# Kernel tuning notes

Hardware: AMD Instinct MI355X
Metric: run time of the kernel (lower is better)

Reference implementation:

```python
import jax, jax.numpy as jnp
import numpy as np


def _glorot(key, shape):
    lim = np.sqrt(6.0 / (shape[-2] + shape[-1])).astype(np.float32)
    return jax.random.uniform(key, shape, jnp.float32, -lim, lim)


def setup_inputs() -> dict:
    key = jax.random.key(0)
    B, F, K, L = 8192, 256, 32768, 4
    H = 2 * F          # CouplingLayer(feat_size, feat_size * 2) hidden width
    half = F // 2      # affine coupling transforms half the features
    ks = jax.random.split(key, 6)
    return {
        "inputs": jax.random.normal(ks[0], (B, F), jnp.float32),
        "W1": _glorot(ks[1], (L, half, H)),
        "b1": jnp.zeros((L, H), jnp.float32),
        "Ws": _glorot(ks[2], (L, H, half)),
        "bs": jnp.zeros((L, half), jnp.float32),
        "Wt": _glorot(ks[3], (L, H, half)),
        "bt": jnp.zeros((L, half), jnp.float32),
        "prior": _glorot(ks[4], (K, F)),  # VQ codebook, GlorotUniform init as in source
    }


def _forward_flow(x, W1, b1, Ws, bs, Wt, bt):
    """Stack of affine coupling layers; returns (y, log|det J|) per sample."""
    L = W1.shape[0]
    jac = jnp.zeros((x.shape[0],), x.dtype)
    for l in range(L):  # small fixed layer count
        xa, xb = jnp.split(x, 2, axis=1)                 # [B, F/2] each
        h = jax.nn.relu(xa @ W1[l] + b1[l])              # [B, 2F]
        s_raw = h @ Ws[l] + bs[l]                        # [B, F/2]
        s = s_raw if l == L - 1 else jnp.tanh(s_raw)     # last layer: tf.identity
        t = h @ Wt[l] + bt[l]
        yb = xb * jnp.exp(s) + t
        jac = jac + jnp.sum(s, axis=1)
        x = jnp.concatenate([yb, xa], axis=1)            # swap halves for mixing
    return x, jac


def reference(inputs, W1, b1, Ws, bs, Wt, bt, prior):
    sg = jax.lax.stop_gradient
    x, jac = _forward_flow(inputs, W1, b1, Ws, bs, Wt, bt)   # [B, F], [B]
    # pairwise squared distance to codebook: [B, K]
    na = jnp.sum(x * x, axis=1, keepdims=True)               # [B, 1]
    nb = jnp.sum(prior * prior, axis=1)[None, :]             # [1, K]
    d = jnp.maximum(na - 2.0 * (x @ prior.T) + nb, 0.0)      # [B, K]
    target_ind = jnp.argmin(d, axis=1)                       # [B]
    target = prior[target_ind]                               # gather, [B, F]
    loss_1 = jnp.mean(jnp.sum((x - sg(target)) ** 2, axis=1) / 2)
    loss_2 = jnp.mean(jnp.sum((sg(x) - target) ** 2, axis=1) / 2)
    loss = loss_1 + 0.25 * loss_2 - jnp.mean(jac)
    return x, loss
```

## Files before the change

kernel.cpp:

```cpp
#include <hip/hip_runtime.h>
#include <hip/hip_fp8.h>
#include <stdint.h>

#define NB     8192
#define NF     256
#define NHALF  128
#define NHID   512
#define NLAY   4
#define NK     32768

#define SX     (1.0f / 16.0f)
#define SP     (256.0f)

typedef __attribute__((ext_vector_type(8))) short bf16x8;
typedef __attribute__((ext_vector_type(4))) float f32x4;
typedef __attribute__((ext_vector_type(8))) int i32x8;

static __device__ __forceinline__ unsigned short f2bf(float f) {
  union { float f; unsigned int u; } v; v.f = f;
  return (unsigned short)((v.u + 0x7FFFu + ((v.u >> 16) & 1u)) >> 16);
}
static __device__ __forceinline__ float bf2f(unsigned short u) {
  union { unsigned int u; float f; } v; v.u = ((unsigned int)u) << 16; return v.f;
}
static __device__ __forceinline__ unsigned char f2fp8(float f) {
  __hip_fp8_e4m3 q(f);
  return (unsigned char)q.__x;
}
static __device__ __forceinline__ float fp82f(unsigned char b) {
  __hip_fp8_e4m3 q; q.__x = b; return (float)q;
}

static __device__ __forceinline__ void load_lds16(const void* g, void* l) {
  __builtin_amdgcn_global_load_lds(
      (const __attribute__((address_space(1))) unsigned int*)g,
      (__attribute__((address_space(3))) unsigned int*)l, 16, 0, 0);
}

static __device__ __forceinline__ unsigned long long packsi(float v, int idx) {
  unsigned int b = __float_as_uint(v);
  b = (b & 0x80000000u) ? ~b : (b | 0x80000000u);
  return ((unsigned long long)b << 32) | (unsigned int)(~(unsigned int)idx);
}

static __device__ __forceinline__ float fast_tanh(float x) {
  const float xc = fminf(fmaxf(x, -15.f), 15.f);
  const float e2 = __expf(2.f * xc);
  return 1.f - 2.f / (e2 + 1.f);
}

static __device__ __forceinline__ int swadr(int kseg, int nrows, int row, int kin) {
  return (kseg * nrows + row) * 64 + (((kin >> 3) ^ (row & 7)) * 8) + (kin & 7);
}

static __device__ __forceinline__ void stage_seg(
    int g, unsigned short* dst,
    const unsigned short* __restrict__ W1T,
    const unsigned short* __restrict__ W2I,
    int wave, int lane, int bxr, int hswap)
{
  const int l = g / 24, s = g % 24;
  const int nc = ((s / 3) + bxr) & 7;
  const int t = s % 3;
  if (t == 0) {
    const unsigned short* W1l = W1T + (size_t)l * (NHID * NHALF) + (size_t)nc * 64 * 128;
#pragma unroll
    for (int u = 0; u < 2; u++) {
      const int chb = (u * 8 + wave) * 64;
      const int ch = chb + lane;
      const int kseg = ch >> 9, cs = ch & 511;
      const int row = cs >> 3, cc = (cs & 7) ^ (row & 7);
      load_lds16(W1l + (size_t)row * 128 + kseg * 64 + cc * 8, dst + chb * 8);
    }
  } else {
    const int half = (t - 1) ^ hswap;
    const unsigned short* W2l = W2I + (size_t)l * (NF * NHID) + nc * 64 + half * 32;
#pragma unroll
    for (int u = 0; u < 2; u++) {
      const int chb = (u * 8 + wave) * 64;
      const int ch = chb + lane;
      const int row = ch >> 2;
      const int cc = (ch & 3) ^ ((row >> 1) & 3);
      load_lds16(W2l + (size_t)row * NHID + cc * 8, dst + chb * 8);
    }
  }
}

__global__ __launch_bounds__(512, 2)
void flow_all(const float* __restrict__ in,
              const unsigned short* __restrict__ W1T,
              const unsigned short* __restrict__ W2I,
              const float* __restrict__ b1A,
              const float* __restrict__ bsA,
              const float* __restrict__ btA,
              float* __restrict__ xout,
              unsigned char* __restrict__ xf8,
              float* __restrict__ jac)
{
  __shared__ __align__(16) unsigned short Xb[2][32 * 128];
  __shared__ __align__(16) unsigned short Hs[32 * 64];
  __shared__ __align__(16) unsigned short Bs[5][8192];
  __shared__ float b1s[NLAY * NHID];
  __shared__ float bss[NLAY * NHALF];
  __shared__ float bts[NLAY * NHALF];
  __shared__ float jlds[4][32];
  const int tid = threadIdx.x;
  const int lane = tid & 63, wave = tid >> 6;
  const int rg = wave >> 2, cg = wave & 3;
  const int q = lane >> 4, c = lane & 15;
  const int m0 = blockIdx.x * 32;
  const int bxr = blockIdx.x & 7;
  const int hswap = (blockIdx.x >> 3) & 1;

  stage_seg(0, Bs[0], W1T, W2I, wave, lane, bxr, hswap);

#pragma unroll
  for (int v = 0; v < 4; v++) {
    const int t4 = tid + v * 512;
    const int row = t4 >> 6, f4 = t4 & 63;
    const float4 d = *(const float4*)(in + (size_t)(m0 + row) * NF + f4 * 4);
    unsigned short* dst = Xb[f4 >> 5];
    const int feat = (f4 & 31) * 4;
    const float vals[4] = {d.x, d.y, d.z, d.w};
#pragma unroll
    for (int u = 0; u < 4; u++) {
      const int fe = feat + u;
      dst[swadr(fe >> 6, 32, row, fe & 63)] = f2bf(vals[u]);
    }
  }

#pragma unroll
  for (int v = 0; v < 4; v++) b1s[tid + v * 512] = b1A[tid + v * 512];
  bss[tid] = bsA[tid];
  bts[tid] = btA[tid];

  stage_seg(1, Bs[1], W1T, W2I, wave, lane, bxr, hswap);
  stage_seg(2, Bs[2], W1T, W2I, wave, lane, bxr, hswap);
  stage_seg(3, Bs[3], W1T, W2I, wave, lane, bxr, hswap);

  float jr[4] = {0.f, 0.f, 0.f, 0.f};
  bf16x8 af1[4];
  const f32x4 z = {0.f, 0.f, 0.f, 0.f};
  f32x4 acc2[4];

  for (int gs = 0; gs < 96; gs++) {
    if (gs < 93)
      asm volatile("s_waitcnt vmcnt(6) lgkmcnt(0)\n\ts_barrier" ::: "memory");
    else if (gs == 93)
      asm volatile("s_waitcnt vmcnt(4) lgkmcnt(0)\n\ts_barrier" ::: "memory");
    else if (gs == 94)
      asm volatile("s_waitcnt vmcnt(2) lgkmcnt(0)\n\ts_barrier" ::: "memory");
    else
      asm volatile("s_waitcnt vmcnt(0) lgkmcnt(0)\n\ts_barrier" ::: "memory");

    if (gs + 4 < 96) stage_seg(gs + 4, Bs[(gs + 4) % 5], W1T, W2I, wave, lane, bxr, hswap);

    const int l = gs / 24, s = gs % 24, typ = s % 3;
    const int nc8 = ((s / 3) + bxr) & 7;
    const unsigned short* B = Bs[gs % 5];
    unsigned short* XA = Xb[l & 1];
    unsigned short* XB = Xb[1 - (l & 1)];

    if (typ == 0) {
      if (s == 0) {
#pragma unroll
        for (int kw = 0; kw < 4; kw++) {
          const int kch = kw * 4 + q;
          af1[kw] = *(const bf16x8*)(XA + ((kch >> 3) * 32 + rg * 16 + c) * 64 +
                                     (((kch & 7) ^ (c & 7)) * 8));
        }
#pragma unroll
        for (int j = 0; j < 4; j++) acc2[j] = z;
      }
      f32x4 acc1 = z;
      const int rb = cg * 16 + c;
#pragma unroll
      for (int kw = 0; kw < 4; kw++) {
        const int kseg = kw >> 1, g = (kw & 1) * 4 + q;
        const bf16x8 bf = *(const bf16x8*)(B + (kseg * 64 + rb) * 64 + ((g ^ (rb & 7)) * 8));
        acc1 = __builtin_amdgcn_mfma_f32_16x16x32_bf16(af1[kw], bf, acc1, 0, 0, 0);
      }
      const int hc = cg * 16 + c;
      const float bb = b1s[l * NHID + nc8 * 64 + hc];
#pragma unroll
      for (int r = 0; r < 4; r++) {
        float v = acc1[r] + bb;
        v = v > 0.f ? v : 0.f;
        Hs[swadr(0, 32, rg * 16 + 4 * q + r, hc)] = f2bf(v);
      }
    } else {
      const int half = (typ - 1) ^ hswap;
      const bf16x8 afh = *(const bf16x8*)(Hs + (rg * 16 + c) * 64 +
                                          (((half * 4 + q) ^ (c & 7)) * 8));
#pragma unroll
      for (int j = 0; j < 4; j++) {
        const int rb = cg * 64 + 16 * j + c;
        const bf16x8 bf = *(const bf16x8*)(B + rb * 32 + ((q ^ ((rb >> 1) & 3)) * 8));
        acc2[j] = __builtin_amdgcn_mfma_f32_16x16x32_bf16(afh, bf, acc2[j], 0, 0, 0);
      }
    }

    if (s == 23) {
      const int parity = c & 1;
      const int lastl = (l == NLAY - 1);
      const float* bsl = bss + l * NHALF;
      const float* btl = bts + l * NHALF;
#pragma unroll
      for (int j = 0; j < 4; j++) {
        const int col = cg * 64 + 16 * j + c;
#pragma unroll
        for (int r = 0; r < 4; r++) {
          const float val = acc2[j][r];
          const float oth = __shfl_xor(val, 1);
          if (!parity) {
            const int feat = col >> 1;
            float sv = val + bsl[feat];
            if (!lastl) sv = fast_tanh(sv);
            const float t = oth + btl[feat];
            const int row = rg * 16 + 4 * q + r;
            const int xaddr = swadr(feat >> 6, 32, row, feat & 63);
            const float xb = bf2f(XB[xaddr]);
            const float yb = xb * __expf(sv) + t;
            jr[r] += sv;
            XB[xaddr] = f2bf(yb);
            if (l >= 2) {
              const int k = lastl ? feat : (NHALF + feat);
              const size_t grow = (size_t)(m0 + row) * NF;
              xout[grow + k] = yb;
              xf8[(size_t)(m0 + row) * 256 + k] = f2fp8(yb * SX);
            }
          }
        }
      }
    }
  }

#pragma unroll
  for (int r = 0; r < 4; r++) {
    float v = jr[r];
    v += __shfl_xor(v, 1); v += __shfl_xor(v, 2);
    v += __shfl_xor(v, 4); v += __shfl_xor(v, 8);
    if (c == 0) jlds[cg][rg * 16 + 4 * q + r] = v;
  }
  __syncthreads();
  if (tid < 32)
    jac[m0 + tid] = jlds[0][tid] + jlds[1][tid] + jlds[2][tid] + jlds[3][tid];
}

__global__ __launch_bounds__(256, 2)
void vq_argmax(const unsigned char* __restrict__ X8,
               const unsigned char* __restrict__ P8,
               const float* __restrict__ nbh,
               unsigned long long* __restrict__ gbest)
{
  __shared__ __align__(16) unsigned char Bs[2][64 * 256];
  const int tid = threadIdx.x;
  const int lane = tid & 63, wave = tid >> 6;
  const int y = blockIdx.x & 15;
  const int m0 = (blockIdx.x >> 4) * 256;
  const int q = lane >> 4, c = lane & 15;
  const int mw = m0 + wave * 64;
  const int one = 0x7F7F7F7F;

  i32x8 af[4][2];
#pragma unroll
  for (int i = 0; i < 4; i++) {
    const unsigned char* xr = X8 + (size_t)(mw + 16 * i + c) * 256 + q * 32;
#pragma unroll
    for (int h = 0; h < 2; h++) {
      const int4 lo = *(const int4*)(xr + h * 128);
      const int4 hi = *(const int4*)(xr + h * 128 + 16);
      af[i][h] = (i32x8){lo.x, lo.y, lo.z, lo.w, hi.x, hi.y, hi.z, hi.w};
    }
  }

  float bestv[16];
  int besti[16];
#pragma unroll
  for (int t = 0; t < 16; t++) { bestv[t] = -1e30f; besti[t] = 0; }

  {
    const int n0s = y * 2048;
#pragma unroll
    for (int u = 0; u < 4; u++) {
      const int chb = (u * 4 + wave) * 64;
      const int ch = chb + lane;
      const int row = ch >> 4, gslot = ch & 15;
      load_lds16(P8 + (size_t)(n0s + row) * 256 + (gslot ^ (row & 15)) * 16,
                 Bs[0] + chb * 16);
    }
  }

  for (int nt = 0; nt < 32; nt++) {
    const int n0 = y * 2048 + nt * 64;
    __syncthreads();

    float nbr[4];
#pragma unroll
    for (int j = 0; j < 4; j++) nbr[j] = nbh[n0 + 16 * j + c];

    if (nt + 1 < 32) {
      const int n0s = n0 + 64;
      unsigned char* dst = Bs[(nt + 1) & 1];
#pragma unroll
      for (int u = 0; u < 4; u++) {
        const int chb = (u * 4 + wave) * 64;
        const int ch = chb + lane;
        const int row = ch >> 4, gslot = ch & 15;
        load_lds16(P8 + (size_t)(n0s + row) * 256 + (gslot ^ (row & 15)) * 16,
                   dst + chb * 16);
      }
    }

    const unsigned char* Bt = Bs[nt & 1];
    f32x4 acc[4][4];
#pragma unroll
    for (int i = 0; i < 4; i++)
#pragma unroll
      for (int j = 0; j < 4; j++)
        acc[i][j] = (f32x4){-nbr[j], -nbr[j], -nbr[j], -nbr[j]};

#pragma unroll
    for (int j = 0; j < 4; j++) {
      const unsigned char* base = Bt + (16 * j + c) * 256;
#pragma unroll
      for (int h = 0; h < 2; h++) {
        const int4 b0 = *(const int4*)(base + ((8 * h + 2 * q)     ^ c) * 16);
        const int4 b1 = *(const int4*)(base + ((8 * h + 2 * q + 1) ^ c) * 16);
        const i32x8 bf = (i32x8){b0.x, b0.y, b0.z, b0.w, b1.x, b1.y, b1.z, b1.w};
#pragma unroll
        for (int i = 0; i < 4; i++)
          acc[i][j] = __builtin_amdgcn_mfma_scale_f32_16x16x128_f8f6f4(
              af[i][h], bf, acc[i][j], 0, 0, 0, one, 0, one);
      }
    }

#pragma unroll
    for (int j = 0; j < 4; j++) {
      const int col = n0 + 16 * j + c;
#pragma unroll
      for (int i = 0; i < 4; i++)
#pragma unroll
        for (int r = 0; r < 4; r++) {
          const float sc = acc[i][j][r];
          const int t = i * 4 + r;
          if (sc > bestv[t]) { bestv[t] = sc; besti[t] = col; }
        }
    }
  }

#pragma unroll
  for (int t = 0; t < 16; t++) {
    float lv = bestv[t]; int li = besti[t];
#pragma unroll
    for (int mk = 8; mk >= 1; mk >>= 1) {
      const float ov = __shfl_xor(lv, mk);
      const int oi = __shfl_xor(li, mk);
      if (ov > lv || (ov == lv && oi < li)) { lv = ov; li = oi; }
    }
    if (c == 0) {
      const int row = mw + 16 * (t >> 2) + q * 4 + (t & 3);
      atomicMax(&gbest[row], packsi(lv, li));
    }
  }
}

__global__ void prep_all(const float* __restrict__ W1,
                         const float* __restrict__ Ws,
                         const float* __restrict__ Wt,
                         const float* __restrict__ prior,
                         unsigned short* __restrict__ W1T,
                         unsigned short* __restrict__ W2I,
                         unsigned char* __restrict__ p8,
                         float* __restrict__ nbh,
                         unsigned long long* __restrict__ gbest,
                         float* __restrict__ accum)
{
  __shared__ float ts[64 * 65];
  const int bx = blockIdx.x;
  const int tid = threadIdx.x;
  if (bx < 2048) {
    const int k = bx * 16 + (tid >> 4);
    const int l16 = tid & 15;
    float s = 0.f;
#pragma unroll
    for (int v = 0; v < 4; v++) {
      const int off = (v * 16 + l16) * 4;
      const float4 d = *(const float4*)(prior + (size_t)k * NF + off);
      uchar4 o;
      o.x = f2fp8(d.x * SP); o.y = f2fp8(d.y * SP);
      o.z = f2fp8(d.z * SP); o.w = f2fp8(d.w * SP);
      *(uchar4*)(p8 + (size_t)k * 256 + off) = o;
      const float q0 = fp82f(o.x), q1 = fp82f(o.y), q2 = fp82f(o.z), q3 = fp82f(o.w);
      s += q0 * q0 + q1 * q1 + q2 * q2 + q3 * q3;
    }
#pragma unroll
    for (int mk = 8; mk >= 1; mk >>= 1) s += __shfl_xor(s, mk);
    if (l16 == 0) nbh[k] = 0.5f * s * (SX / SP);
  } else if (bx < 2112) {
    const int job = bx - 2048;
    const int l = job >> 4, t = job & 15;
    const int k0 = (t >> 3) * 64, n0 = (t & 7) * 64;
    const float* src = W1 + (size_t)l * NHALF * NHID;
#pragma unroll
    for (int v = 0; v < 16; v++) {
      const int e = tid + v * 256;
      const int kk = e >> 6, nn = e & 63;
      ts[kk * 65 + nn] = src[(size_t)(k0 + kk) * NHID + n0 + nn];
    }
    __syncthreads();
    unsigned short* dst = W1T + (size_t)l * NHID * NHALF;
#pragma unroll
    for (int v = 0; v < 16; v++) {
      const int e = tid + v * 256;
      const int nn = e >> 6, kk = e & 63;
      dst[(size_t)(n0 + nn) * NHALF + k0 + kk] = f2bf(ts[kk * 65 + nn]);
    }
  } else if (bx < 2240) {
    const int job = bx - 2112;
    const int l = job >> 5, rem = job & 31;
    const int b = rem >> 4;
    const int k0 = ((rem >> 1) & 7) * 64;
    const int f0 = (rem & 1) * 64;
    const float* src = (b ? Wt : Ws) + (size_t)l * NHID * NHALF;
#pragma unroll
    for (int v = 0; v < 16; v++) {
      const int e = tid + v * 256;
      const int kk = e >> 6, nn = e & 63;
      ts[kk * 65 + nn] = src[(size_t)(k0 + kk) * NHALF + f0 + nn];
    }
    __syncthreads();
#pragma unroll
    for (int v = 0; v < 16; v++) {
      const int e = tid + v * 256;
      const int nn = e >> 6, kk = e & 63;
      W2I[((size_t)l * NF + 2 * (f0 + nn) + b) * NHID + k0 + kk] = f2bf(ts[kk * 65 + nn]);
    }
  } else {
    const int idx = (bx - 2240) * 256 + tid;
    if (idx < NB) gbest[idx] = 0ull;
    if (idx < 4) accum[idx] = 0.f;
  }
}

__global__ void vq_finalize(const float* __restrict__ X,
                            const float* __restrict__ prior,
                            const unsigned long long* __restrict__ gbest,
                            const float* __restrict__ jac,
                            float* __restrict__ accum,
                            float* __restrict__ loss)
{
  const int wave = threadIdx.x >> 6, lane = threadIdx.x & 63;
  const int gw = blockIdx.x * 4 + wave;
  float accd = 0.f, accj = 0.f;
  for (int r = 0; r < 8; r++) {
    const int row = gw * 8 + r;
    const unsigned int idx = ~(unsigned int)(gbest[row]);
    const float* x = X + (size_t)row * NF;
    const float* p = prior + (size_t)idx * NF;
#pragma unroll
    for (int u = 0; u < 4; u++) {
      const int d = lane + u * 64;
      const float df = x[d] - p[d];
      accd += df * df;
    }
    if (lane == 0) accj += jac[row];
  }
#pragma unroll
  for (int mk = 32; mk >= 1; mk >>= 1) {
    accd += __shfl_xor(accd, mk);
    accj += __shfl_xor(accj, mk);
  }
  __shared__ float sd[4], sj[4];
  if (lane == 0) { sd[wave] = accd; sj[wave] = accj; }
  __syncthreads();
  if (threadIdx.x == 0) {
    atomicAdd(&accum[0], sd[0] + sd[1] + sd[2] + sd[3]);
    atomicAdd(&accum[1], sj[0] + sj[1] + sj[2] + sj[3]);
    __threadfence();
    const unsigned int t = atomicAdd((unsigned int*)&accum[2], 1u);
    if (t == 255u) {
      const float d = atomicAdd(&accum[0], 0.f);
      const float jv = atomicAdd(&accum[1], 0.f);
      loss[0] = 1.25f * (0.5f * d / (float)NB) - jv / (float)NB;
    }
  }
}

extern "C" void kernel_launch(void* const* d_in, const int* in_sizes, int n_in,
                              void* d_out, int out_size, void* d_ws, size_t ws_size,
                              hipStream_t stream)
{
  (void)in_sizes; (void)n_in; (void)out_size; (void)ws_size;
  const float* inputs = (const float*)d_in[0];
  const float* W1 = (const float*)d_in[1];
  const float* b1 = (const float*)d_in[2];
  const float* Ws = (const float*)d_in[3];
  const float* bs = (const float*)d_in[4];
  const float* Wt = (const float*)d_in[5];
  const float* bt = (const float*)d_in[6];
  const float* prior = (const float*)d_in[7];

  char* p = (char*)d_ws;
  auto alloc = [&](size_t bytes) { char* r = p; p += (bytes + 255) & ~(size_t)255; return r; };
  unsigned short* W1T  = (unsigned short*)alloc((size_t)NLAY * NHID * NHALF * 2);
  unsigned short* W2I  = (unsigned short*)alloc((size_t)NLAY * NF * NHID * 2);
  unsigned char* P8    = (unsigned char*)alloc((size_t)NK * 256);
  float* NBH           = (float*)alloc((size_t)NK * 4);
  unsigned char* XF8   = (unsigned char*)alloc((size_t)NB * 256);
  float* JAC           = (float*)alloc((size_t)NB * 4);
  unsigned long long* GBEST = (unsigned long long*)alloc((size_t)NB * 8);
  float* ACC           = (float*)alloc(256);

  float* xout = (float*)d_out;
  float* loss = xout + (size_t)NB * NF;

  prep_all<<<dim3(2272), 256, 0, stream>>>(
      W1, Ws, Wt, prior, W1T, W2I, P8, NBH, GBEST, ACC);

  flow_all<<<dim3(NB / 32), 512, 0, stream>>>(
      inputs, W1T, W2I, b1, bs, bt, xout, XF8, JAC);

  vq_argmax<<<dim3(32 * 16), 256, 0, stream>>>(XF8, P8, NBH, GBEST);
  vq_finalize<<<dim3(256), 256, 0, stream>>>(xout, prior, GBEST, JAC, ACC, loss);
}
```

Before: 257.0 us.

## Fuse hidden-layer GEMMs in registers via transposed MFMA, coarsen weight staging

Computes the first GEMM transposed (weights as the A operand, activations as B) so each lane's output fragment can be packed directly into the A operand of the second GEMM. This removes the Hs shared-memory round trip and the step that split the second GEMM into halves. The 96 fine-grained steps become 32 chunks, each staging the W1 block and the full W2 block together. Buffering changes from a 5-deep ring to a double buffer with an extra barrier per chunk. The cost is less prefetch depth and more LDS per stage.

```diff
diff --git a/kernel.cpp b/kernel.cpp
--- a/kernel.cpp
+++ b/kernel.cpp
@@ -53,36 +53,32 @@
   return (kseg * nrows + row) * 64 + (((kin >> 3) ^ (row & 7)) * 8) + (kin & 7);
 }
 
-static __device__ __forceinline__ void stage_seg(
+static __device__ __forceinline__ int g1swz(int row) {
+  return (row & 15) ^ ((row & 8) >> 1);
+}
+
+static __device__ __forceinline__ void stage_chunk(
     int g, unsigned short* dst,
     const unsigned short* __restrict__ W1T,
     const unsigned short* __restrict__ W2I,
-    int wave, int lane, int bxr, int hswap)
+    int wave, int lane, int bxr)
 {
-  const int l = g / 24, s = g % 24;
-  const int nc = ((s / 3) + bxr) & 7;
-  const int t = s % 3;
-  if (t == 0) {
-    const unsigned short* W1l = W1T + (size_t)l * (NHID * NHALF) + (size_t)nc * 64 * 128;
-#pragma unroll
-    for (int u = 0; u < 2; u++) {
-      const int chb = (u * 8 + wave) * 64;
-      const int ch = chb + lane;
-      const int kseg = ch >> 9, cs = ch & 511;
-      const int row = cs >> 3, cc = (cs & 7) ^ (row & 7);
-      load_lds16(W1l + (size_t)row * 128 + kseg * 64 + cc * 8, dst + chb * 8);
-    }
-  } else {
-    const int half = (t - 1) ^ hswap;
-    const unsigned short* W2l = W2I + (size_t)l * (NF * NHID) + nc * 64 + half * 32;
-#pragma unroll
-    for (int u = 0; u < 2; u++) {
-      const int chb = (u * 8 + wave) * 64;
-      const int ch = chb + lane;
-      const int row = ch >> 2;
-      const int cc = (ch & 3) ^ ((row >> 1) & 3);
-      load_lds16(W2l + (size_t)row * NHID + cc * 8, dst + chb * 8);
-    }
+  const int l = g >> 3;
+  const int nc = ((g & 7) + bxr) & 7;
+  const unsigned short* W1l = W1T + (size_t)l * (NHID * NHALF) + (size_t)nc * 64 * 128;
+#pragma unroll
+  for (int u = 0; u < 2; u++) {
+    const int ch = (u * 8 + wave) * 64 + lane;
+    const int row = ch >> 4, sl = ch & 15;
+    load_lds16(W1l + (size_t)row * 128 + (sl ^ g1swz(row)) * 8, dst + ch * 8);
+  }
+  const unsigned short* W2l = W2I + (size_t)l * (NF * NHID) + nc * 64;
+#pragma unroll
+  for (int u = 0; u < 4; u++) {
+    const int ch = (u * 8 + wave) * 64 + lane;
+    const int col = ch >> 3, sl = ch & 7;
+    load_lds16(W2l + (size_t)col * NHID + ((sl ^ (col & 7)) * 8),
+               dst + 8192 + ch * 8);
   }
 }
 
@@ -98,8 +94,7 @@
               float* __restrict__ jac)
 {
   __shared__ __align__(16) unsigned short Xb[2][32 * 128];
-  __shared__ __align__(16) unsigned short Hs[32 * 64];
-  __shared__ __align__(16) unsigned short Bs[5][8192];
+  __shared__ __align__(16) unsigned short Bs[2][24576];
   __shared__ float b1s[NLAY * NHID];
   __shared__ float bss[NLAY * NHALF];
   __shared__ float bts[NLAY * NHALF];
@@ -110,9 +105,8 @@
   const int q = lane >> 4, c = lane & 15;
   const int m0 = blockIdx.x * 32;
   const int bxr = blockIdx.x & 7;
-  const int hswap = (blockIdx.x >> 3) & 1;
-
-  stage_seg(0, Bs[0], W1T, W2I, wave, lane, bxr, hswap);
+
+  stage_chunk(0, Bs[0], W1T, W2I, wave, lane, bxr);
 
 #pragma unroll
   for (int v = 0; v < 4; v++) {
@@ -134,73 +128,70 @@
   bss[tid] = bsA[tid];
   bts[tid] = btA[tid];
 
-  stage_seg(1, Bs[1], W1T, W2I, wave, lane, bxr, hswap);
-  stage_seg(2, Bs[2], W1T, W2I, wave, lane, bxr, hswap);
-  stage_seg(3, Bs[3], W1T, W2I, wave, lane, bxr, hswap);
+  stage_chunk(1, Bs[1], W1T, W2I, wave, lane, bxr);
 
   float jr[4] = {0.f, 0.f, 0.f, 0.f};
   bf16x8 af1[4];
   const f32x4 z = {0.f, 0.f, 0.f, 0.f};
   f32x4 acc2[4];
 
-  for (int gs = 0; gs < 96; gs++) {
-    if (gs < 93)
+  for (int g = 0; g < 32; g++) {
+    if (g < 31)
       asm volatile("s_waitcnt vmcnt(6) lgkmcnt(0)\n\ts_barrier" ::: "memory");
-    else if (gs == 93)
-      asm volatile("s_waitcnt vmcnt(4) lgkmcnt(0)\n\ts_barrier" ::: "memory");
-    else if (gs == 94)
-      asm volatile("s_waitcnt vmcnt(2) lgkmcnt(0)\n\ts_barrier" ::: "memory");
     else
       asm volatile("s_waitcnt vmcnt(0) lgkmcnt(0)\n\ts_barrier" ::: "memory");
 
-    if (gs + 4 < 96) stage_seg(gs + 4, Bs[(gs + 4) % 5], W1T, W2I, wave, lane, bxr, hswap);
-
-    const int l = gs / 24, s = gs % 24, typ = s % 3;
-    const int nc8 = ((s / 3) + bxr) & 7;
-    const unsigned short* B = Bs[gs % 5];
+    const int l = g >> 3, s = g & 7;
+    const int nc = (s + bxr) & 7;
+    const unsigned short* B = Bs[g & 1];
+    const unsigned short* W2B = B + 8192;
     unsigned short* XA = Xb[l & 1];
     unsigned short* XB = Xb[1 - (l & 1)];
 
-    if (typ == 0) {
-      if (s == 0) {
-#pragma unroll
-        for (int kw = 0; kw < 4; kw++) {
-          const int kch = kw * 4 + q;
-          af1[kw] = *(const bf16x8*)(XA + ((kch >> 3) * 32 + rg * 16 + c) * 64 +
-                                     (((kch & 7) ^ (c & 7)) * 8));
+    if (s == 0) {
+#pragma unroll
+      for (int kw = 0; kw < 4; kw++) {
+        const int kch = kw * 4 + q;
+        af1[kw] = *(const bf16x8*)(XA + ((kch >> 3) * 32 + rg * 16 + c) * 64 +
+                                   (((kch & 7) ^ (c & 7)) * 8));
+      }
+#pragma unroll
+      for (int j = 0; j < 4; j++) acc2[j] = z;
+    }
+
+    const int bias_base = l * NHID + nc * 64;
+#pragma unroll
+    for (int P = 0; P < 2; P++) {
+      union { unsigned int u[4]; bf16x8 v; } a2;
+#pragma unroll
+      for (int tb = 0; tb < 2; tb++) {
+        f32x4 acc1 = z;
+        const int row = P * 32 + 8 * (c >> 2) + (c & 3) + 4 * tb;
+        const int gsw = g1swz(row);
+#pragma unroll
+        for (int kk = 0; kk < 4; kk++) {
+          const bf16x8 a1 = *(const bf16x8*)(B + row * 128 +
+                                             (((kk * 4 + q) ^ gsw) * 8));
+          acc1 = __builtin_amdgcn_mfma_f32_16x16x32_bf16(a1, af1[kk], acc1, 0, 0, 0);
         }
-#pragma unroll
-        for (int j = 0; j < 4; j++) acc2[j] = z;
+        const float4 bb = *(const float4*)(b1s + bias_base + P * 32 + 8 * q + 4 * tb);
+        const float v0 = fmaxf(acc1[0] + bb.x, 0.f);
+        const float v1 = fmaxf(acc1[1] + bb.y, 0.f);
+        const float v2 = fmaxf(acc1[2] + bb.z, 0.f);
+        const float v3 = fmaxf(acc1[3] + bb.w, 0.f);
+        a2.u[tb * 2]     = (unsigned int)f2bf(v0) | ((unsigned int)f2bf(v1) << 16);
+        a2.u[tb * 2 + 1] = (unsigned int)f2bf(v2) | ((unsigned int)f2bf(v3) << 16);
       }
-      f32x4 acc1 = z;
-      const int rb = cg * 16 + c;
-#pragma unroll
-      for (int kw = 0; kw < 4; kw++) {
-        const int kseg = kw >> 1, g = (kw & 1) * 4 + q;
-        const bf16x8 bf = *(const bf16x8*)(B + (kseg * 64 + rb) * 64 + ((g ^ (rb & 7)) * 8));
-        acc1 = __builtin_amdgcn_mfma_f32_16x16x32_bf16(af1[kw], bf, acc1, 0, 0, 0);
+#pragma unroll
+      for (int j = 0; j < 4; j++) {
+        const int col = cg * 64 + 16 * j + c;
+        const bf16x8 b2 = *(const bf16x8*)(W2B + col * 64 +
+                                           (((P * 4 + q) ^ (col & 7)) * 8));
+        acc2[j] = __builtin_amdgcn_mfma_f32_16x16x32_bf16(a2.v, b2, acc2[j], 0, 0, 0);
       }
-      const int hc = cg * 16 + c;
-      const float bb = b1s[l * NHID + nc8 * 64 + hc];
-#pragma unroll
-      for (int r = 0; r < 4; r++) {
-        float v = acc1[r] + bb;
-        v = v > 0.f ? v : 0.f;
-        Hs[swadr(0, 32, rg * 16 + 4 * q + r, hc)] = f2bf(v);
-      }
-    } else {
-      const int half = (typ - 1) ^ hswap;
-      const bf16x8 afh = *(const bf16x8*)(Hs + (rg * 16 + c) * 64 +
-                                          (((half * 4 + q) ^ (c & 7)) * 8));
-#pragma unroll
-      for (int j = 0; j < 4; j++) {
-        const int rb = cg * 64 + 16 * j + c;
-        const bf16x8 bf = *(const bf16x8*)(B + rb * 32 + ((q ^ ((rb >> 1) & 3)) * 8));
-        acc2[j] = __builtin_amdgcn_mfma_f32_16x16x32_bf16(afh, bf, acc2[j], 0, 0, 0);
-      }
-    }
-
-    if (s == 23) {
+    }
+
+    if (s == 7) {
       const int parity = c & 1;
       const int lastl = (l == NLAY - 1);
       const float* bsl = bss + l * NHALF;
@@ -233,6 +224,9 @@
         }
       }
     }
+
+    asm volatile("s_waitcnt lgkmcnt(0)\n\ts_barrier" ::: "memory");
+    if (g + 2 < 32) stage_chunk(g + 2, Bs[g & 1], W1T, W2I, wave, lane, bxr);
   }
 
 #pragma unroll
```

Result: faster. 237.4 us (-7.6%).
